# Kernel tuning notes

Hardware: AMD Instinct MI355X
Metric: run time of the kernel (lower is better)

The kernel has to match this reference:

```python
import jax, jax.numpy as jnp
import numpy as np

B, C, H, W = 32, 384, 28, 28
E, HID, K = 4, 384, 2  # HID = hidden_features(1536) // num_experts(4)


def setup_inputs() -> dict:
    key = jax.random.key(0)
    ks = jax.random.split(key, 5)
    x = jax.random.normal(ks[0], (B, C, H, W), jnp.float32)
    gate_w = jax.random.normal(ks[1], (C, E), jnp.float32) * 0.02
    gate_b = jnp.zeros((E,), jnp.float32)
    w1 = jax.random.normal(ks[2], (E, HID, C), jnp.float32) * 0.02
    b1 = jnp.zeros((E, HID), jnp.float32)
    w2 = jax.random.normal(ks[3], (E, C, HID), jnp.float32) * 0.02
    b2 = jnp.zeros((E, C), jnp.float32)
    return {"x": x, "gate_w": gate_w, "gate_b": gate_b,
            "w1": w1, "b1": b1, "w2": w2, "b2": b2}


def reference(x, gate_w, gate_b, w1, b1, w2, b2):
    b, c, h, w = x.shape
    e = gate_b.shape[0]
    # per-token gating: tokens are spatial positions in NHWC order
    x_flat = x.transpose(0, 2, 3, 1).reshape(-1, c)          # [N, C], N = B*H*W
    scores = jax.nn.softmax(x_flat @ gate_w + gate_b, -1)    # [N, E]
    top_v, top_i = jax.lax.top_k(scores, K)                  # [N, K]
    top_w = jax.nn.softmax(top_v, -1)                        # [N, K] renormalized
    # weight map per top-k slot: [K, B, H, W]
    wmap = top_w.T.reshape(K, b, h, w)
    # faithful to torch loop: expert i contributes at slot k iff ANY token routed
    # to it at slot k; the weight applied is the UNMASKED slot-k weight map.
    present = (top_i[:, :, None] == jnp.arange(e)[None, None, :]).any(0)  # [K, E]
    coef = jnp.einsum('ke,kbhw->ebhw', present.astype(x.dtype), wmap)     # [E, B, H, W]
    # dense per-expert 1x1-conv MLP over the FULL tensor (as in the source)
    hdn = jax.nn.relu(jnp.einsum('bchw,edc->ebdhw', x, w1)
                      + b1[:, None, :, None, None])          # [E, B, HID, H, W]
    y = jnp.einsum('ebdhw,eod->ebohw', hdn, w2) + b2[:, None, :, None, None]
    out = jnp.einsum('ebohw,ebhw->bohw', y, coef)            # [B, C, H, W]
    return out
```

## Files before the change

### kernel.cpp

```cpp
#include <hip/hip_runtime.h>
#include <hip/hip_bf16.h>
#include <stdint.h>

#define B_DIM 32
#define C_DIM 384
#define HW_DIM 784
#define E_DIM 4
#define HID_DIM 384
#define NTOK (B_DIM * HW_DIM)
#define NH (E_DIM * HID_DIM)

using short8 = __attribute__((ext_vector_type(8))) short;
using f32x4  = __attribute__((ext_vector_type(4))) float;
typedef unsigned short ushort_t;

__device__ __forceinline__ ushort_t f2bf(float f) {
  __hip_bfloat16 h = __float2bfloat16(f);
  return __builtin_bit_cast(ushort_t, h);
}

__device__ __forceinline__ void gload_lds16(const void* g, void* l) {
  __builtin_amdgcn_global_load_lds(
      (const __attribute__((address_space(1))) unsigned int*)g,
      (__attribute__((address_space(3))) unsigned int*)l, 16, 0, 0);
}

__global__ __launch_bounds__(256) void prep_kernel(
    const float* __restrict__ w1, const float* __restrict__ w2,
    ushort_t* __restrict__ W1b, ushort_t* __restrict__ W2b,
    unsigned int* __restrict__ present) {
  int i = blockIdx.x * 256 + threadIdx.x;
  if (i == 0) *present = 0u;
  if (i < NH * C_DIM) {
    W1b[i] = f2bf(w1[i]);
    int o = i / NH;
    int r = i - o * NH;
    int e = r / HID_DIM;
    int k = r - e * HID_DIM;
    W2b[i] = f2bf(w2[((size_t)e * C_DIM + o) * HID_DIM + k]);
  }
}

__global__ __launch_bounds__(256) void gate_kernel(
    const float* __restrict__ x, const float* __restrict__ gw,
    const float* __restrict__ gb, ushort_t* __restrict__ xb,
    float* __restrict__ topw, unsigned int* __restrict__ present) {
  __shared__ __align__(16) ushort_t lxs[64][392];
  __shared__ float pscore[4][64][4];
  __shared__ unsigned int pmask;
  const int b = blockIdx.x;
  const int p0 = blockIdx.y * 64;
  const int cnt = min(64, HW_DIM - p0);
  const int tid = threadIdx.x;
  const int cg = tid >> 6, tl = tid & 63;
  if (tid == 0) pmask = 0u;
  float a0 = 0.f, a1 = 0.f, a2 = 0.f, a3 = 0.f;
  const bool valid = tl < cnt;
  if (valid) {
    const float* xp = x + (size_t)b * C_DIM * HW_DIM + p0 + tl;
    for (int c = cg; c < C_DIM; c += 4) {
      const float v = xp[(size_t)c * HW_DIM];
      lxs[tl][c] = f2bf(v);
      const float4 g = *(const float4*)&gw[c * 4];
      a0 += v * g.x; a1 += v * g.y; a2 += v * g.z; a3 += v * g.w;
    }
  }
  pscore[cg][tl][0] = a0; pscore[cg][tl][1] = a1;
  pscore[cg][tl][2] = a2; pscore[cg][tl][3] = a3;
  __syncthreads();
  if (cg == 0 && valid) {
    float z[4];
#pragma unroll
    for (int e = 0; e < 4; e++)
      z[e] = pscore[0][tl][e] + pscore[1][tl][e] + pscore[2][tl][e] +
             pscore[3][tl][e] + gb[e];
    const float mx = fmaxf(fmaxf(z[0], z[1]), fmaxf(z[2], z[3]));
    float s[4]; float sum = 0.f;
#pragma unroll
    for (int e = 0; e < 4; e++) { s[e] = __expf(z[e] - mx); sum += s[e]; }
    const float inv = 1.f / sum;
#pragma unroll
    for (int e = 0; e < 4; e++) s[e] *= inv;
    int e0 = 0; float v0 = s[0];
#pragma unroll
    for (int e = 1; e < 4; e++) if (s[e] > v0) { v0 = s[e]; e0 = e; }
    int e1 = -1; float v1 = -1.f;
#pragma unroll
    for (int e = 0; e < 4; e++) if (e != e0 && s[e] > v1) { v1 = s[e]; e1 = e; }
    const float r = __expf(v1 - v0);
    const float w0 = 1.f / (1.f + r);
    const int m = b * HW_DIM + p0 + tl;
    topw[m * 2] = w0;
    topw[m * 2 + 1] = 1.f - w0;
    atomicOr(&pmask, (1u << e0) | (1u << (4 + e1)));
  }
  __syncthreads();
  if (tid == 0) atomicOr(present, pmask);
  const int nchunk = cnt * 48;
  for (int ci = tid; ci < nchunk; ci += 256) {
    const int row = ci / 48, c8 = ci - row * 48;
    short8 v = *(const short8*)&lxs[row][c8 * 8];
    *(short8*)&xb[(size_t)(b * HW_DIM + p0 + row) * C_DIM + c8 * 8] = v;
  }
}

template <int KDIM, int EPI>
__global__ __launch_bounds__(256, 3) void gemm64(
    const ushort_t* __restrict__ A, const ushort_t* __restrict__ Bw,
    const float* __restrict__ bias, const float* __restrict__ topw,
    const unsigned int* __restrict__ presentp,
    ushort_t* __restrict__ hOut, float* __restrict__ outp) {
  constexpr int BM = 64, BN = 128, BK = 64;
  constexpr int KT = KDIM / BK;
  constexpr int NTN = (EPI == 0 ? NH / BN : C_DIM / BN);
  constexpr int ASZ = BM * BK;
  constexpr int BSZ = BN * BK;
  __shared__ ushort_t smem[2 * ASZ + 2 * BSZ];

  const int nwg = NTN * (NTOK / BM);
  const int orig = blockIdx.x;
  const int xcd = orig & 7;
  const int qq = nwg >> 3, rr = nwg & 7;
  const int wg = (xcd < rr ? xcd * (qq + 1) : rr * (qq + 1) + (xcd - rr) * qq)
               + (orig >> 3);
  const int mt = wg / NTN, nt = wg % NTN;
  const int m0 = mt * BM, n0 = nt * BN;

  const int tid = threadIdx.x;
  const int lane = tid & 63;
  const int wid = tid >> 6;
  const int wm = wid >> 1, wn = wid & 1;

  auto stage = [&](int t) {
    ushort_t* dstA = smem + (t & 1) * ASZ;
    ushort_t* dstB = smem + 2 * ASZ + (t & 1) * BSZ;
    const int kb = t * BK;
#pragma unroll
    for (int li = 0; li < 2; ++li) {
      const int P = (li * 256 + tid) * 16;
      const int row = P >> 7;
      const int cb = (P & 127) ^ ((row & 7) << 4);
      gload_lds16(&A[(size_t)(m0 + row) * KDIM + kb + (cb >> 1)],
                  (char*)dstA + P);
    }
#pragma unroll
    for (int li = 0; li < 4; ++li) {
      const int P = (li * 256 + tid) * 16;
      const int row = P >> 7;
      const int cb = (P & 127) ^ ((row & 7) << 4);
      gload_lds16(&Bw[(size_t)(n0 + row) * KDIM + kb + (cb >> 1)],
                  (char*)dstB + P);
    }
  };

  f32x4 acc[2][4] = {};

  stage(0);
  stage(1);
  for (int t = 0; t < KT; ++t) {
    if (t + 1 < KT)
      asm volatile("s_waitcnt vmcnt(6)" ::: "memory");
    else
      asm volatile("s_waitcnt vmcnt(0)" ::: "memory");
    __builtin_amdgcn_sched_barrier(0);
    __builtin_amdgcn_s_barrier();
    __builtin_amdgcn_sched_barrier(0);
    const char* Ab = (const char*)(smem + (t & 1) * ASZ);
    const char* Bb = (const char*)(smem + 2 * ASZ + (t & 1) * BSZ);
    short8 av[2][2], bv[4][2];
#pragma unroll
    for (int i = 0; i < 2; ++i)
#pragma unroll
      for (int kk = 0; kk < 2; ++kk) {
        const int row = wm * 32 + i * 16 + (lane & 15);
        const int cb = (kk * 64 + ((lane >> 4) * 16)) ^ ((row & 7) << 4);
        av[i][kk] = *(const short8*)(Ab + row * 128 + cb);
      }
#pragma unroll
    for (int i = 0; i < 4; ++i)
#pragma unroll
      for (int kk = 0; kk < 2; ++kk) {
        const int row = wn * 64 + i * 16 + (lane & 15);
        const int cb = (kk * 64 + ((lane >> 4) * 16)) ^ ((row & 7) << 4);
        bv[i][kk] = *(const short8*)(Bb + row * 128 + cb);
      }
    __builtin_amdgcn_s_setprio(1);
#pragma unroll
    for (int kk = 0; kk < 2; ++kk)
#pragma unroll
      for (int i = 0; i < 2; ++i)
#pragma unroll
        for (int j = 0; j < 4; ++j)
          acc[i][j] = __builtin_amdgcn_mfma_f32_16x16x32_bf16(
              av[i][kk], bv[j][kk], acc[i][j], 0, 0, 0);
    __builtin_amdgcn_s_setprio(0);
    __builtin_amdgcn_sched_barrier(0);
    __builtin_amdgcn_s_barrier();
    __builtin_amdgcn_sched_barrier(0);
    if (t + 2 < KT) stage(t + 2);
  }

  const unsigned int pm = *presentp;
  if constexpr (EPI == 0) {
    ushort_t* tr = smem;
    const int e = n0 / HID_DIM;
    const float P0 = (float)((pm >> e) & 1u);
    const float P1 = (float)((pm >> (4 + e)) & 1u);
#pragma unroll
    for (int mi = 0; mi < 2; ++mi) {
      const int r0 = wm * 32 + mi * 16 + (lane >> 4) * 4;
      const int mg = m0 + r0;
      const float4 t0 = *(const float4*)&topw[mg * 2];
      const float4 t1 = *(const float4*)&topw[mg * 2 + 4];
      const float cj[4] = {P0 * t0.x + P1 * t0.y, P0 * t0.z + P1 * t0.w,
                           P0 * t1.x + P1 * t1.y, P0 * t1.z + P1 * t1.w};
#pragma unroll
      for (int ni = 0; ni < 4; ++ni) {
        const int cl = wn * 64 + ni * 16 + (lane & 15);
        const float bvv = bias[n0 + cl];
#pragma unroll
        for (int j = 0; j < 4; ++j) {
          float v = fmaxf(acc[mi][ni][j] + bvv, 0.f);
          tr[(r0 + j) * 128 + cl] = f2bf(cj[j] * v);
        }
      }
    }
    __syncthreads();
#pragma unroll
    for (int it = 0; it < 4; ++it) {
      const int c = it * 256 + tid;
      const int row = c >> 4, cr = c & 15;
      *(short8*)&hOut[(size_t)(m0 + row) * NH + n0 + cr * 8] =
          *(const short8*)&tr[row * 128 + cr * 8];
    }
  } else {
    float B0[4], B1[4];
#pragma unroll
    for (int ni = 0; ni < 4; ++ni) {
      const int o = n0 + wn * 64 + ni * 16 + (lane & 15);
      float s0 = 0.f, s1 = 0.f;
#pragma unroll
      for (int e2 = 0; e2 < 4; ++e2) {
        const float bb = bias[e2 * C_DIM + o];
        s0 += (float)((pm >> e2) & 1u) * bb;
        s1 += (float)((pm >> (4 + e2)) & 1u) * bb;
      }
      B0[ni] = s0; B1[ni] = s1;
    }
#pragma unroll
    for (int mi = 0; mi < 2; ++mi) {
      const int mg = m0 + wm * 32 + mi * 16 + (lane >> 4) * 4;
      const float4 t0 = *(const float4*)&topw[mg * 2];
      const float4 t1 = *(const float4*)&topw[mg * 2 + 4];
      const int bb2 = mg / HW_DIM;
      const int p = mg - bb2 * HW_DIM;
#pragma unroll
      for (int ni = 0; ni < 4; ++ni) {
        const int o = n0 + wn * 64 + ni * 16 + (lane & 15);
        float4 v;
        v.x = acc[mi][ni][0] + t0.x * B0[ni] + t0.y * B1[ni];
        v.y = acc[mi][ni][1] + t0.z * B0[ni] + t0.w * B1[ni];
        v.z = acc[mi][ni][2] + t1.x * B0[ni] + t1.y * B1[ni];
        v.w = acc[mi][ni][3] + t1.z * B0[ni] + t1.w * B1[ni];
        *(float4*)&outp[((size_t)bb2 * C_DIM + o) * HW_DIM + p] = v;
      }
    }
  }
}

extern "C" void kernel_launch(void* const* d_in, const int* in_sizes, int n_in,
                              void* d_out, int out_size, void* d_ws, size_t ws_size,
                              hipStream_t stream) {
  const float* x  = (const float*)d_in[0];
  const float* gw = (const float*)d_in[1];
  const float* gb = (const float*)d_in[2];
  const float* w1 = (const float*)d_in[3];
  const float* b1 = (const float*)d_in[4];
  const float* w2 = (const float*)d_in[5];
  const float* b2 = (const float*)d_in[6];
  float* out = (float*)d_out;

  char* ws = (char*)d_ws;
  ushort_t* xb = (ushort_t*)ws;   ws += (size_t)NTOK * C_DIM * 2;
  ushort_t* hdnS = (ushort_t*)ws; ws += (size_t)NTOK * NH * 2;
  ushort_t* W1b = (ushort_t*)ws;  ws += (size_t)NH * C_DIM * 2;
  ushort_t* W2b = (ushort_t*)ws;  ws += (size_t)C_DIM * NH * 2;
  float* topw = (float*)ws;       ws += (size_t)NTOK * 2 * 4;
  unsigned int* present = (unsigned int*)ws;

  prep_kernel<<<dim3((NH * C_DIM) / 256), dim3(256), 0, stream>>>(
      w1, w2, W1b, W2b, present);
  gate_kernel<<<dim3(B_DIM, 13), dim3(256), 0, stream>>>(
      x, gw, gb, xb, topw, present);
  gemm64<C_DIM, 0><<<dim3((NTOK / 64) * (NH / 128)), dim3(256), 0, stream>>>(
      xb, W1b, b1, topw, present, hdnS, nullptr);
  gemm64<NH, 1><<<dim3((NTOK / 64) * (C_DIM / 128)), dim3(256), 0, stream>>>(
      hdnS, W2b, b2, topw, present, nullptr, out);
}
```

Baseline: 131.0 us.

## Retile GEMMs to BK=32 with 128-row tiles for GEMM1 and 2-wave GEMM2

Both GEMMs are rebuilt around a K-step of 32 with a 64-byte LDS row swizzle. Each wave now computes a 64x64 output block (4x4 MFMA tiles), which doubles register accumulators per wave. GEMM1 uses 128x128 tiles with 4 waves and occupancy hint 5. GEMM2 keeps 64x128 tiles but runs only 2 waves per block. The aim is better operand reuse per wave and smaller LDS footprint for higher occupancy, at the cost of twice as many barrier-synchronised K iterations and fewer waves per block in GEMM2.

After: 249.5 us. +90.5%, slower.

```diff
diff --git a/kernel.cpp b/kernel.cpp
--- a/kernel.cpp
+++ b/kernel.cpp
@@ -104,17 +104,23 @@
   }
 }
 
-template <int KDIM, int EPI>
-__global__ __launch_bounds__(256, 3) void gemm64(
+template <int KDIM, int BM, int EPI>
+__global__ __launch_bounds__(BM == 128 ? 256 : 128, BM == 128 ? 5 : 3)
+void gemm_k32(
     const ushort_t* __restrict__ A, const ushort_t* __restrict__ Bw,
     const float* __restrict__ bias, const float* __restrict__ topw,
     const unsigned int* __restrict__ presentp,
     ushort_t* __restrict__ hOut, float* __restrict__ outp) {
-  constexpr int BM = 64, BN = 128, BK = 64;
+  constexpr int BN = 128, BK = 32;
   constexpr int KT = KDIM / BK;
+  constexpr int NTHR = (BM == 128 ? 256 : 128);
+  constexpr int MR = 4;
   constexpr int NTN = (EPI == 0 ? NH / BN : C_DIM / BN);
   constexpr int ASZ = BM * BK;
   constexpr int BSZ = BN * BK;
+  constexpr int NLA = BM * BK * 2 / (NTHR * 16);
+  constexpr int NLB = BN * BK * 2 / (NTHR * 16);
+  constexpr int L = NLA + NLB;
   __shared__ ushort_t smem[2 * ASZ + 2 * BSZ];
 
   const int nwg = NTN * (NTOK / BM);
@@ -129,70 +135,64 @@
   const int tid = threadIdx.x;
   const int lane = tid & 63;
   const int wid = tid >> 6;
-  const int wm = wid >> 1, wn = wid & 1;
+  const int wm = (BM == 128) ? (wid >> 1) : 0;
+  const int wn = (BM == 128) ? (wid & 1) : wid;
+  const int lanel = lane & 15, laneq = lane >> 4;
 
   auto stage = [&](int t) {
     ushort_t* dstA = smem + (t & 1) * ASZ;
     ushort_t* dstB = smem + 2 * ASZ + (t & 1) * BSZ;
     const int kb = t * BK;
 #pragma unroll
-    for (int li = 0; li < 2; ++li) {
-      const int P = (li * 256 + tid) * 16;
-      const int row = P >> 7;
-      const int cb = (P & 127) ^ ((row & 7) << 4);
+    for (int li = 0; li < NLA; ++li) {
+      const int P = (li * NTHR + tid) * 16;
+      const int row = P >> 6;
+      const int cb = (P & 63) ^ ((row & 3) << 4);
       gload_lds16(&A[(size_t)(m0 + row) * KDIM + kb + (cb >> 1)],
                   (char*)dstA + P);
     }
 #pragma unroll
-    for (int li = 0; li < 4; ++li) {
-      const int P = (li * 256 + tid) * 16;
-      const int row = P >> 7;
-      const int cb = (P & 127) ^ ((row & 7) << 4);
+    for (int li = 0; li < NLB; ++li) {
+      const int P = (li * NTHR + tid) * 16;
+      const int row = P >> 6;
+      const int cb = (P & 63) ^ ((row & 3) << 4);
       gload_lds16(&Bw[(size_t)(n0 + row) * KDIM + kb + (cb >> 1)],
                   (char*)dstB + P);
     }
   };
 
-  f32x4 acc[2][4] = {};
+  f32x4 acc[MR][4] = {};
+  const int cbr = (laneq * 16) ^ ((lanel & 3) << 4);
 
   stage(0);
   stage(1);
   for (int t = 0; t < KT; ++t) {
-    if (t + 1 < KT)
-      asm volatile("s_waitcnt vmcnt(6)" ::: "memory");
-    else
+    if (t + 1 < KT) {
+      if constexpr (L == 4)
+        asm volatile("s_waitcnt vmcnt(4)" ::: "memory");
+      else
+        asm volatile("s_waitcnt vmcnt(6)" ::: "memory");
+    } else {
       asm volatile("s_waitcnt vmcnt(0)" ::: "memory");
+    }
     __builtin_amdgcn_sched_barrier(0);
     __builtin_amdgcn_s_barrier();
     __builtin_amdgcn_sched_barrier(0);
-    const char* Ab = (const char*)(smem + (t & 1) * ASZ);
-    const char* Bb = (const char*)(smem + 2 * ASZ + (t & 1) * BSZ);
-    short8 av[2][2], bv[4][2];
-#pragma unroll
-    for (int i = 0; i < 2; ++i)
-#pragma unroll
-      for (int kk = 0; kk < 2; ++kk) {
-        const int row = wm * 32 + i * 16 + (lane & 15);
-        const int cb = (kk * 64 + ((lane >> 4) * 16)) ^ ((row & 7) << 4);
-        av[i][kk] = *(const short8*)(Ab + row * 128 + cb);
-      }
-#pragma unroll
-    for (int i = 0; i < 4; ++i)
-#pragma unroll
-      for (int kk = 0; kk < 2; ++kk) {
-        const int row = wn * 64 + i * 16 + (lane & 15);
-        const int cb = (kk * 64 + ((lane >> 4) * 16)) ^ ((row & 7) << 4);
-        bv[i][kk] = *(const short8*)(Bb + row * 128 + cb);
-      }
+    const char* Ab = (const char*)(smem + (t & 1) * ASZ) + (wm * 64 + lanel) * 64;
+    const char* Bb = (const char*)(smem + 2 * ASZ + (t & 1) * BSZ) +
+                     (wn * 64 + lanel) * 64;
+    short8 av[MR], bv[4];
+#pragma unroll
+    for (int i = 0; i < MR; ++i) av[i] = *(const short8*)(Ab + i * 1024 + cbr);
+#pragma unroll
+    for (int j = 0; j < 4; ++j) bv[j] = *(const short8*)(Bb + j * 1024 + cbr);
     __builtin_amdgcn_s_setprio(1);
 #pragma unroll
-    for (int kk = 0; kk < 2; ++kk)
-#pragma unroll
-      for (int i = 0; i < 2; ++i)
-#pragma unroll
-        for (int j = 0; j < 4; ++j)
-          acc[i][j] = __builtin_amdgcn_mfma_f32_16x16x32_bf16(
-              av[i][kk], bv[j][kk], acc[i][j], 0, 0, 0);
+    for (int i = 0; i < MR; ++i)
+#pragma unroll
+      for (int j = 0; j < 4; ++j)
+        acc[i][j] = __builtin_amdgcn_mfma_f32_16x16x32_bf16(
+            av[i], bv[j], acc[i][j], 0, 0, 0);
     __builtin_amdgcn_s_setprio(0);
     __builtin_amdgcn_sched_barrier(0);
     __builtin_amdgcn_s_barrier();
@@ -202,13 +202,14 @@
 
   const unsigned int pm = *presentp;
   if constexpr (EPI == 0) {
+    __syncthreads();
     ushort_t* tr = smem;
     const int e = n0 / HID_DIM;
     const float P0 = (float)((pm >> e) & 1u);
     const float P1 = (float)((pm >> (4 + e)) & 1u);
 #pragma unroll
-    for (int mi = 0; mi < 2; ++mi) {
-      const int r0 = wm * 32 + mi * 16 + (lane >> 4) * 4;
+    for (int mi = 0; mi < MR; ++mi) {
+      const int r0 = wm * 64 + mi * 16 + laneq * 4;
       const int mg = m0 + r0;
       const float4 t0 = *(const float4*)&topw[mg * 2];
       const float4 t1 = *(const float4*)&topw[mg * 2 + 4];
@@ -216,7 +217,7 @@
                            P0 * t1.x + P1 * t1.y, P0 * t1.z + P1 * t1.w};
 #pragma unroll
       for (int ni = 0; ni < 4; ++ni) {
-        const int cl = wn * 64 + ni * 16 + (lane & 15);
+        const int cl = wn * 64 + ni * 16 + lanel;
         const float bvv = bias[n0 + cl];
 #pragma unroll
         for (int j = 0; j < 4; ++j) {
@@ -227,8 +228,8 @@
     }
     __syncthreads();
 #pragma unroll
-    for (int it = 0; it < 4; ++it) {
-      const int c = it * 256 + tid;
+    for (int it = 0; it < BM * 16 / NTHR; ++it) {
+      const int c = it * NTHR + tid;
       const int row = c >> 4, cr = c & 15;
       *(short8*)&hOut[(size_t)(m0 + row) * NH + n0 + cr * 8] =
           *(const short8*)&tr[row * 128 + cr * 8];
@@ -237,7 +238,7 @@
     float B0[4], B1[4];
 #pragma unroll
     for (int ni = 0; ni < 4; ++ni) {
-      const int o = n0 + wn * 64 + ni * 16 + (lane & 15);
+      const int o = n0 + wn * 64 + ni * 16 + lanel;
       float s0 = 0.f, s1 = 0.f;
 #pragma unroll
       for (int e2 = 0; e2 < 4; ++e2) {
@@ -248,15 +249,15 @@
       B0[ni] = s0; B1[ni] = s1;
     }
 #pragma unroll
-    for (int mi = 0; mi < 2; ++mi) {
-      const int mg = m0 + wm * 32 + mi * 16 + (lane >> 4) * 4;
+    for (int mi = 0; mi < MR; ++mi) {
+      const int mg = m0 + wm * 64 + mi * 16 + laneq * 4;
       const float4 t0 = *(const float4*)&topw[mg * 2];
       const float4 t1 = *(const float4*)&topw[mg * 2 + 4];
       const int bb2 = mg / HW_DIM;
       const int p = mg - bb2 * HW_DIM;
 #pragma unroll
       for (int ni = 0; ni < 4; ++ni) {
-        const int o = n0 + wn * 64 + ni * 16 + (lane & 15);
+        const int o = n0 + wn * 64 + ni * 16 + lanel;
         float4 v;
         v.x = acc[mi][ni][0] + t0.x * B0[ni] + t0.y * B1[ni];
         v.y = acc[mi][ni][1] + t0.z * B0[ni] + t0.w * B1[ni];
@@ -292,8 +293,10 @@
       w1, w2, W1b, W2b, present);
   gate_kernel<<<dim3(B_DIM, 13), dim3(256), 0, stream>>>(
       x, gw, gb, xb, topw, present);
-  gemm64<C_DIM, 0><<<dim3((NTOK / 64) * (NH / 128)), dim3(256), 0, stream>>>(
-      xb, W1b, b1, topw, present, hdnS, nullptr);
-  gemm64<NH, 1><<<dim3((NTOK / 64) * (C_DIM / 128)), dim3(256), 0, stream>>>(
-      hdnS, W2b, b2, topw, present, nullptr, out);
-}
+  gemm_k32<C_DIM, 128, 0>
+      <<<dim3((NTOK / 128) * (NH / 128)), dim3(256), 0, stream>>>(
+          xb, W1b, b1, topw, present, hdnS, nullptr);
+  gemm_k32<NH, 64, 1>
+      <<<dim3((NTOK / 64) * (C_DIM / 128)), dim3(128), 0, stream>>>(
+          hdnS, W2b, b2, topw, present, nullptr, out);
+}
```
